# Performance work log

Hardware: AMD Instinct MI355X
Metric: run time of the kernel (lower is better)

## Reference

```python
import jax, jax.numpy as jnp
import numpy as np

RX, RY = 8, 2
ANGLES = [0, 90]
M_DIM = N_DIM = 2048


def _make_kernel(rx=RX, ry=RY, angles=ANGLES):
    # Faithful reproduction of GuidedFilterJAX.__init__ kernel construction.
    # For angles that are multiples of 90 deg, scipy ndimage.rotate(order=2,
    # reshape=False) on a square array is exactly np.rot90.
    kernelL = []
    for A in angles:
        k = np.zeros((rx * 4 + 1, rx * 4 + 1), dtype=np.float32)
        if ry == 0:
            k[:, rx * 2] = 1.0
        else:
            k[:, rx * 2 - ry: rx * 2 + ry + 1] = 1.0
        if A % 360 != 0:
            k = np.rot90(k, (A // 90) % 4)
        k = k[rx:3 * rx + 1, rx:3 * rx + 1]
        r = int((k.sum(1) != 0).sum()) // 2 * 2
        c = int((k.sum(0) != 0).sum()) // 2 * 2
        kernelL.append(k[rx - r // 2: rx + r // 2 + 1,
                         rx - c // 2: rx + c // 2 + 1][None, None])
    C = max(kk.shape[-2] for kk in kernelL)
    R = max(kk.shape[-1] for kk in kernelL)
    out = np.zeros((len(angles), 1, C, R), dtype=np.float32)
    for i, kk in enumerate(kernelL):
        dc = (C - kk.shape[-2]) // 2
        dr = (R - kk.shape[-1]) // 2
        out[i, :, dc:dc + kk.shape[-2], dr:dr + kk.shape[-1]] = kk[0, 0]
    return out


def setup_inputs() -> dict:
    key = jax.random.key(0)
    k1, k2 = jax.random.split(key)
    X = jax.random.normal(k1, (1, 1, M_DIM, N_DIM), dtype=jnp.float32)
    y = jax.random.normal(k2, (1, 1, M_DIM, N_DIM), dtype=jnp.float32)
    kernel = jnp.asarray(_make_kernel())  # (AngleNum, 1, c, r)
    return {"X": X, "y": y, "kernel": kernel}


def _boxfilter(x, k, pc, pr):
    # zero-pad then grouped VALID conv (feature_group_count = channels = 1)
    xp = jnp.pad(x, ((0, 0), (0, 0), (pc, pc), (pr, pr)))
    return jax.lax.conv_general_dilated(xp, k, (1, 1), 'VALID',
                                        feature_group_count=x.shape[1])


def reference(X, y, kernel):
    pr, pc = kernel.shape[-1] // 2, kernel.shape[-2] // 2
    ones = jnp.ones_like(X)
    for i in range(kernel.shape[0]):  # small fixed loop over angles
        k = kernel[i:i + 1]
        Ni = _boxfilter(ones, k, pc, pr)          # normalizer (precomputed in orig)
        mean_y = _boxfilter(y, k, pc, pr) / Ni
        mean_x = _boxfilter(X, k, pc, pr) / Ni
        X = X + (mean_y - mean_x)
    return X
```

## Files before the change

kernel.cpp:

```cpp
#include <hip/hip_runtime.h>

#define W 2048
#define H 2048
#define TX 64
#define TY 32
#define HALO 10
#define DW 84
#define DH 52
#define VW 84
#define VH 36

typedef float f4 __attribute__((ext_vector_type(4)));
typedef float f2 __attribute__((ext_vector_type(2)));

__global__ __launch_bounds__(512, 6) void guided_fused(const float* __restrict__ X,
                                                       const float* __restrict__ y,
                                                       float* __restrict__ out) {
    __shared__ float Ds[DH * DW];
    __shared__ float Vs[VH * VW];

    const int tid = threadIdx.x;
    const int i0 = blockIdx.y * TY;
    const int j0 = blockIdx.x * TX;

    for (int c = tid; c < DH * 21; c += 512) {
        int li = c / 21, k4 = (c - li * 21) * 4;
        int gi = i0 + li - HALO;
        int gj = j0 + k4 - HALO;
        f4 d = {0.f, 0.f, 0.f, 0.f};
        if ((unsigned)gi < H) {
            const float* yp = &y[gi * W + gj];
            const float* xp = &X[gi * W + gj];
            if (gj >= 0 && gj + 3 < W) {
                f2 ya = *(const f2*)yp, yb = *(const f2*)(yp + 2);
                f2 xa = *(const f2*)xp, xb = *(const f2*)(xp + 2);
                d = (f4){ya.x - xa.x, ya.y - xa.y, yb.x - xb.x, yb.y - xb.y};
            } else {
                #pragma unroll
                for (int e = 0; e < 4; ++e) {
                    int g = gj + e;
                    if ((unsigned)g < W) d[e] = yp[e] - xp[e];
                }
            }
        }
        *(f4*)&Ds[li * DW + k4] = d;
    }
    __syncthreads();

    if (tid < 189) {
        int grp = tid % 21, seg = tid / 21;
        int jj = grp * 4, v0 = seg * 4;
        const f4* dp = (const f4*)&Ds[v0 * DW + jj];
        #define DROW(t) dp[(t) * (DW / 4)]
        f4 r0 = DROW(0), r1 = DROW(1), r2 = DROW(2);
        f4 s = r0 + r1 + r2;
        #pragma unroll
        for (int t = 3; t < 17; ++t) s += DROW(t);
        f4* vp = (f4*)&Vs[v0 * VW + jj];
        vp[0] = s;
        s += DROW(17) - r0; vp[VW / 4] = s;
        s += DROW(18) - r1; vp[2 * (VW / 4)] = s;
        s += DROW(19) - r2; vp[3 * (VW / 4)] = s;
        #undef DROW
    }
    __syncthreads();

    for (int c = tid; c < VH * 20; c += 512) {
        int v = c / 20, g4 = (c - v * 20) * 4;
        int gi = i0 + v - 2;
        if ((unsigned)gi >= H) continue;
        f4 a = *(const f4*)&Vs[v * VW + g4];
        f4 b = *(const f4*)&Vs[v * VW + g4 + 4];
        float m = a.y + a.z + a.w + b.x;
        float s0 = m + a.x;
        float s1 = m + b.y;
        float s2 = a.z + a.w + b.x + b.y + b.z;
        float s3 = a.w + b.x + b.y + b.z + b.w;
        int r0 = gi - 8 > 0 ? gi - 8 : 0, r1 = gi + 8 < H - 1 ? gi + 8 : H - 1;
        float rowsN = (float)(r1 - r0 + 1);
        float corr[4] = {s0, s1, s2, s3};
        #pragma unroll
        for (int k = 0; k < 4; ++k) {
            int gj = j0 + g4 + k - 8;
            if ((unsigned)gj < W) {
                int c0 = gj - 2 > 0 ? gj - 2 : 0, c1 = gj + 2 < W - 1 ? gj + 2 : W - 1;
                corr[k] *= __builtin_amdgcn_rcpf(rowsN * (float)(c1 - c0 + 1));
            } else {
                corr[k] = 0.f;
            }
        }
        int off = (v + 8) * DW + g4 + 2;
        f2 o01 = *(f2*)&Ds[off];
        f2 o23 = *(f2*)&Ds[off + 2];
        o01.x -= corr[0]; o01.y -= corr[1];
        o23.x -= corr[2]; o23.y -= corr[3];
        *(f2*)&Ds[off] = o01;
        *(f2*)&Ds[off + 2] = o23;
    }
    __syncthreads();

    if (tid < 160) {
        int grp = tid % 20, seg = tid / 20;
        int g4 = grp * 4, w0 = seg * 4;
        const float* base = &Ds[(w0 + 8) * DW + g4 + 2];
        #define D2ROW(t) ({ f2 p_ = *(const f2*)&base[(t) * DW]; \
                            f2 q_ = *(const f2*)&base[(t) * DW + 2]; \
                            (f4){p_.x, p_.y, q_.x, q_.y}; })
        f4 r0 = D2ROW(0), r1 = D2ROW(1), r2 = D2ROW(2);
        f4 s = r0 + r1 + r2 + D2ROW(3) + D2ROW(4);
        f4* vp = (f4*)&Vs[w0 * VW + g4];
        vp[0] = s;
        s += D2ROW(5) - r0; vp[VW / 4] = s;
        s += D2ROW(6) - r1; vp[2 * (VW / 4)] = s;
        s += D2ROW(7) - r2; vp[3 * (VW / 4)] = s;
        #undef D2ROW
    }
    __syncthreads();

    {
        int w = tid >> 4, x0 = (tid & 15) * 4;
        int gi = i0 + w;
        int r0 = gi - 2 > 0 ? gi - 2 : 0, r1 = gi + 2 < H - 1 ? gi + 2 : H - 1;
        float rowsN = (float)(r1 - r0 + 1);
        float val[20];
        #pragma unroll
        for (int q = 0; q < 5; ++q) {
            f4 t = *(const f4*)&Vs[w * VW + x0 + q * 4];
            val[q * 4 + 0] = t.x; val[q * 4 + 1] = t.y;
            val[q * 4 + 2] = t.z; val[q * 4 + 3] = t.w;
        }
        float s = 0.f;
        #pragma unroll
        for (int c = 0; c < 17; ++c) s += val[c];
        float f[4];
        #pragma unroll
        for (int x = 0; x < 4; ++x) {
            int gj = j0 + x0 + x;
            int c0 = gj - 8 > 0 ? gj - 8 : 0, c1 = gj + 8 < W - 1 ? gj + 8 : W - 1;
            f[x] = s * __builtin_amdgcn_rcpf(rowsN * (float)(c1 - c0 + 1));
            if (x < 3) s += val[x + 17] - val[x];
        }
        int off = (w + 10) * DW + (x0 + 10);
        f2 o01 = *(f2*)&Ds[off];
        f2 o23 = *(f2*)&Ds[off + 2];
        o01.x = f[0] - o01.x; o01.y = f[1] - o01.y;
        o23.x = f[2] - o23.x; o23.y = f[3] - o23.y;
        *(f2*)&Ds[off] = o01;
        *(f2*)&Ds[off + 2] = o23;
    }
    __syncthreads();

    {
        int w = tid >> 4, g = tid & 15;
        int gi = i0 + w, gj = j0 + 4 * g;
        int b = (w + 10) * DW + 4 * g + 10;
        f2 p = *(const f2*)&Ds[b], q = *(const f2*)&Ds[b + 2];
        f4 yv = *(const f4*)&y[gi * W + gj];
        f4 o = {yv.x + p.x, yv.y + p.y, yv.z + q.x, yv.w + q.y};
        *(f4*)&out[gi * W + gj] = o;
    }
}

extern "C" void kernel_launch(void* const* d_in, const int* in_sizes, int n_in,
                              void* d_out, int out_size, void* d_ws, size_t ws_size,
                              hipStream_t stream) {
    const float* X = (const float*)d_in[0];
    const float* y = (const float*)d_in[1];
    float* out = (float*)d_out;

    dim3 blk(512, 1, 1);
    dim3 grd(W / TX, H / TY, 1);
    guided_fused<<<grd, blk, 0, stream>>>(X, y, out);
}
```

Measured before the change: 94.68 us.

## Align halo loads to 16 bytes and add interior fast path with constant normalizer

Result: faster. 90.55 us (-4.4%).

```diff
diff --git a/kernel.cpp b/kernel.cpp
--- a/kernel.cpp
+++ b/kernel.cpp
@@ -4,160 +4,180 @@
 #define H 2048
 #define TX 64
 #define TY 32
-#define HALO 10
-#define DW 84
+#define DW 92
 #define DH 52
-#define VW 84
 #define VH 36
 
 typedef float f4 __attribute__((ext_vector_type(4)));
-typedef float f2 __attribute__((ext_vector_type(2)));
 
-__global__ __launch_bounds__(512, 6) void guided_fused(const float* __restrict__ X,
+__global__ __launch_bounds__(512, 8) void guided_fused(const float* __restrict__ X,
                                                        const float* __restrict__ y,
                                                        float* __restrict__ out) {
-    __shared__ float Ds[DH * DW];
-    __shared__ float Vs[VH * VW];
+    __shared__ __align__(16) float Ds[DH * DW];
+    __shared__ __align__(16) float Vs[VH * DW];
 
     const int tid = threadIdx.x;
-    const int i0 = blockIdx.y * TY;
-    const int j0 = blockIdx.x * TX;
+    const int bx = blockIdx.x, by = blockIdx.y;
+    const int i0 = by * TY, j0 = bx * TX;
+    const bool interior = (bx >= 1) & (bx <= 30) & (by >= 1) & (by <= 62);
+    const float R85 = 0.011764706f;
 
-    for (int c = tid; c < DH * 21; c += 512) {
-        int li = c / 21, k4 = (c - li * 21) * 4;
-        int gi = i0 + li - HALO;
-        int gj = j0 + k4 - HALO;
-        f4 d = {0.f, 0.f, 0.f, 0.f};
-        if ((unsigned)gi < H) {
-            const float* yp = &y[gi * W + gj];
-            const float* xp = &X[gi * W + gj];
-            if (gj >= 0 && gj + 3 < W) {
-                f2 ya = *(const f2*)yp, yb = *(const f2*)(yp + 2);
-                f2 xa = *(const f2*)xp, xb = *(const f2*)(xp + 2);
-                d = (f4){ya.x - xa.x, ya.y - xa.y, yb.x - xb.x, yb.y - xb.y};
+    if (interior) {
+        #pragma unroll
+        for (int k = 0; k < 3; ++k) {
+            int c = tid + k * 512;
+            if (c < DH * 22) {
+                int li = c / 22, g = c - li * 22;
+                int off = (i0 - 10 + li) * W + (j0 - 12) + 4 * g;
+                f4 yv = *(const f4*)&y[off];
+                f4 xv = *(const f4*)&X[off];
+                *(f4*)&Ds[li * DW + 4 * g] = yv - xv;
+            }
+        }
+    } else {
+        #pragma unroll
+        for (int k = 0; k < 3; ++k) {
+            int c = tid + k * 512;
+            if (c < DH * 22) {
+                int li = c / 22, g = c - li * 22;
+                int gi = i0 - 10 + li, gj = j0 - 12 + 4 * g;
+                f4 d = {0.f, 0.f, 0.f, 0.f};
+                if ((unsigned)gi < H) {
+                    if (gj >= 0 && gj + 3 < W) {
+                        f4 yv = *(const f4*)&y[gi * W + gj];
+                        f4 xv = *(const f4*)&X[gi * W + gj];
+                        d = yv - xv;
+                    } else {
+                        #pragma unroll
+                        for (int e = 0; e < 4; ++e) {
+                            int gc = gj + e;
+                            if ((unsigned)gc < W) d[e] = y[gi * W + gc] - X[gi * W + gc];
+                        }
+                    }
+                }
+                *(f4*)&Ds[li * DW + 4 * g] = d;
+            }
+        }
+    }
+    __syncthreads();
+
+    if (tid < 198) {
+        int seg = tid / 22, g = tid - seg * 22;
+        int v0 = seg * 4;
+        const f4* dp = (const f4*)&Ds[v0 * DW + 4 * g];
+        f4 r0 = dp[0], r1 = dp[23], r2 = dp[46];
+        f4 s = r0 + r1 + r2;
+        #pragma unroll
+        for (int t = 3; t < 17; ++t) s += dp[t * 23];
+        f4* vp = (f4*)&Vs[v0 * DW + 4 * g];
+        vp[0] = s;
+        s += dp[17 * 23] - r0; vp[23] = s;
+        s += dp[18 * 23] - r1; vp[46] = s;
+        s += dp[19 * 23] - r2; vp[69] = s;
+    }
+    __syncthreads();
+
+    #pragma unroll
+    for (int k = 0; k < 2; ++k) {
+        int c = tid + k * 512;
+        if (c < VH * 21) {
+            int v = c / 21, t = c - v * 21;
+            f4 a = *(const f4*)&Vs[v * DW + 4 * t];
+            f4 b = *(const f4*)&Vs[v * DW + 4 * t + 4];
+            float m = a.y + a.z + a.w + b.x;
+            float s0 = m + a.x;
+            float s1 = m + b.y;
+            float s2 = a.z + a.w + b.x + b.y + b.z;
+            float s3 = a.w + b.x + b.y + b.z + b.w;
+            int off = (v + 8) * DW + 4 * t + 2;
+            if (interior) {
+                Ds[off + 0] -= s0 * R85;
+                Ds[off + 1] -= s1 * R85;
+                Ds[off + 2] -= s2 * R85;
+                Ds[off + 3] -= s3 * R85;
             } else {
-                #pragma unroll
-                for (int e = 0; e < 4; ++e) {
-                    int g = gj + e;
-                    if ((unsigned)g < W) d[e] = yp[e] - xp[e];
+                int gi = i0 + v - 2;
+                if ((unsigned)gi < H) {
+                    int r0c = gi - 8 > 0 ? gi - 8 : 0;
+                    int r1c = gi + 8 < H - 1 ? gi + 8 : H - 1;
+                    float rowsN = (float)(r1c - r0c + 1);
+                    float corr[4] = {s0, s1, s2, s3};
+                    #pragma unroll
+                    for (int e = 0; e < 4; ++e) {
+                        int gj = j0 - 10 + 4 * t + e;
+                        if ((unsigned)gj < W) {
+                            int c0 = gj - 2 > 0 ? gj - 2 : 0;
+                            int c1 = gj + 2 < W - 1 ? gj + 2 : W - 1;
+                            corr[e] *= __builtin_amdgcn_rcpf(rowsN * (float)(c1 - c0 + 1));
+                        } else {
+                            corr[e] = 0.f;
+                        }
+                        Ds[off + e] -= corr[e];
+                    }
                 }
             }
         }
-        *(f4*)&Ds[li * DW + k4] = d;
     }
     __syncthreads();
 
-    if (tid < 189) {
-        int grp = tid % 21, seg = tid / 21;
-        int jj = grp * 4, v0 = seg * 4;
-        const f4* dp = (const f4*)&Ds[v0 * DW + jj];
-        #define DROW(t) dp[(t) * (DW / 4)]
-        f4 r0 = DROW(0), r1 = DROW(1), r2 = DROW(2);
-        f4 s = r0 + r1 + r2;
-        #pragma unroll
-        for (int t = 3; t < 17; ++t) s += DROW(t);
-        f4* vp = (f4*)&Vs[v0 * VW + jj];
+    if (tid < 320) {
+        int seg = tid / 20, g = tid - seg * 20;
+        int w0 = seg * 2;
+        int lc = 4 * g + 4;
+        const f4* dp = (const f4*)&Ds[(w0 + 8) * DW + lc];
+        f4 r0 = dp[0];
+        f4 s = r0 + dp[23] + dp[46] + dp[69] + dp[92];
+        f4* vp = (f4*)&Vs[w0 * DW + lc];
         vp[0] = s;
-        s += DROW(17) - r0; vp[VW / 4] = s;
-        s += DROW(18) - r1; vp[2 * (VW / 4)] = s;
-        s += DROW(19) - r2; vp[3 * (VW / 4)] = s;
-        #undef DROW
-    }
-    __syncthreads();
-
-    for (int c = tid; c < VH * 20; c += 512) {
-        int v = c / 20, g4 = (c - v * 20) * 4;
-        int gi = i0 + v - 2;
-        if ((unsigned)gi >= H) continue;
-        f4 a = *(const f4*)&Vs[v * VW + g4];
-        f4 b = *(const f4*)&Vs[v * VW + g4 + 4];
-        float m = a.y + a.z + a.w + b.x;
-        float s0 = m + a.x;
-        float s1 = m + b.y;
-        float s2 = a.z + a.w + b.x + b.y + b.z;
-        float s3 = a.w + b.x + b.y + b.z + b.w;
-        int r0 = gi - 8 > 0 ? gi - 8 : 0, r1 = gi + 8 < H - 1 ? gi + 8 : H - 1;
-        float rowsN = (float)(r1 - r0 + 1);
-        float corr[4] = {s0, s1, s2, s3};
-        #pragma unroll
-        for (int k = 0; k < 4; ++k) {
-            int gj = j0 + g4 + k - 8;
-            if ((unsigned)gj < W) {
-                int c0 = gj - 2 > 0 ? gj - 2 : 0, c1 = gj + 2 < W - 1 ? gj + 2 : W - 1;
-                corr[k] *= __builtin_amdgcn_rcpf(rowsN * (float)(c1 - c0 + 1));
-            } else {
-                corr[k] = 0.f;
-            }
-        }
-        int off = (v + 8) * DW + g4 + 2;
-        f2 o01 = *(f2*)&Ds[off];
-        f2 o23 = *(f2*)&Ds[off + 2];
-        o01.x -= corr[0]; o01.y -= corr[1];
-        o23.x -= corr[2]; o23.y -= corr[3];
-        *(f2*)&Ds[off] = o01;
-        *(f2*)&Ds[off + 2] = o23;
-    }
-    __syncthreads();
-
-    if (tid < 160) {
-        int grp = tid % 20, seg = tid / 20;
-        int g4 = grp * 4, w0 = seg * 4;
-        const float* base = &Ds[(w0 + 8) * DW + g4 + 2];
-        #define D2ROW(t) ({ f2 p_ = *(const f2*)&base[(t) * DW]; \
-                            f2 q_ = *(const f2*)&base[(t) * DW + 2]; \
-                            (f4){p_.x, p_.y, q_.x, q_.y}; })
-        f4 r0 = D2ROW(0), r1 = D2ROW(1), r2 = D2ROW(2);
-        f4 s = r0 + r1 + r2 + D2ROW(3) + D2ROW(4);
-        f4* vp = (f4*)&Vs[w0 * VW + g4];
-        vp[0] = s;
-        s += D2ROW(5) - r0; vp[VW / 4] = s;
-        s += D2ROW(6) - r1; vp[2 * (VW / 4)] = s;
-        s += D2ROW(7) - r2; vp[3 * (VW / 4)] = s;
-        #undef D2ROW
+        s += dp[115] - r0; vp[23] = s;
     }
     __syncthreads();
 
     {
         int w = tid >> 4, x0 = (tid & 15) * 4;
-        int gi = i0 + w;
-        int r0 = gi - 2 > 0 ? gi - 2 : 0, r1 = gi + 2 < H - 1 ? gi + 2 : H - 1;
-        float rowsN = (float)(r1 - r0 + 1);
         float val[20];
+        const f4* vp = (const f4*)&Vs[w * DW + x0 + 4];
         #pragma unroll
         for (int q = 0; q < 5; ++q) {
-            f4 t = *(const f4*)&Vs[w * VW + x0 + q * 4];
-            val[q * 4 + 0] = t.x; val[q * 4 + 1] = t.y;
-            val[q * 4 + 2] = t.z; val[q * 4 + 3] = t.w;
+            f4 tq = vp[q];
+            val[q * 4 + 0] = tq.x; val[q * 4 + 1] = tq.y;
+            val[q * 4 + 2] = tq.z; val[q * 4 + 3] = tq.w;
         }
         float s = 0.f;
         #pragma unroll
         for (int c = 0; c < 17; ++c) s += val[c];
-        float f[4];
-        #pragma unroll
-        for (int x = 0; x < 4; ++x) {
-            int gj = j0 + x0 + x;
-            int c0 = gj - 8 > 0 ? gj - 8 : 0, c1 = gj + 8 < W - 1 ? gj + 8 : W - 1;
-            f[x] = s * __builtin_amdgcn_rcpf(rowsN * (float)(c1 - c0 + 1));
-            if (x < 3) s += val[x + 17] - val[x];
+        f4 d2 = *(const f4*)&Ds[(w + 10) * DW + x0 + 12];
+        int gbase = (i0 + w) * W + j0 + x0;
+        f4 yv = *(const f4*)&y[gbase];
+        f4 o;
+        if (interior) {
+            o.x = yv.x - d2.x + s * R85;
+            s += val[17] - val[0];
+            o.y = yv.y - d2.y + s * R85;
+            s += val[18] - val[1];
+            o.z = yv.z - d2.z + s * R85;
+            s += val[19] - val[2];
+            o.w = yv.w - d2.w + s * R85;
+        } else {
+            int gi = i0 + w;
+            int r0c = gi - 2 > 0 ? gi - 2 : 0;
+            int r1c = gi + 2 < H - 1 ? gi + 2 : H - 1;
+            float rowsN = (float)(r1c - r0c + 1);
+            float res[4];
+            #pragma unroll
+            for (int e = 0; e < 4; ++e) {
+                int gj = j0 + x0 + e;
+                int c0 = gj - 8 > 0 ? gj - 8 : 0;
+                int c1 = gj + 8 < W - 1 ? gj + 8 : W - 1;
+                res[e] = s * __builtin_amdgcn_rcpf(rowsN * (float)(c1 - c0 + 1));
+                if (e < 3) s += val[e + 17] - val[e];
+            }
+            o.x = yv.x - d2.x + res[0];
+            o.y = yv.y - d2.y + res[1];
+            o.z = yv.z - d2.z + res[2];
+            o.w = yv.w - d2.w + res[3];
         }
-        int off = (w + 10) * DW + (x0 + 10);
-        f2 o01 = *(f2*)&Ds[off];
-        f2 o23 = *(f2*)&Ds[off + 2];
-        o01.x = f[0] - o01.x; o01.y = f[1] - o01.y;
-        o23.x = f[2] - o23.x; o23.y = f[3] - o23.y;
-        *(f2*)&Ds[off] = o01;
-        *(f2*)&Ds[off + 2] = o23;
-    }
-    __syncthreads();
-
-    {
-        int w = tid >> 4, g = tid & 15;
-        int gi = i0 + w, gj = j0 + 4 * g;
-        int b = (w + 10) * DW + 4 * g + 10;
-        f2 p = *(const f2*)&Ds[b], q = *(const f2*)&Ds[b + 2];
-        f4 yv = *(const f4*)&y[gi * W + gj];
-        f4 o = {yv.x + p.x, yv.y + p.y, yv.z + q.x, yv.w + q.y};
-        *(f4*)&out[gi * W + gj] = o;
+        *(f4*)&out[gbase] = o;
     }
 }
 
```
